# Optimization experiments

Measured on AMD Instinct MI355X. Metric: run time of the kernel, lower is better.

The kernel has to match this reference:

```python
import jax, jax.numpy as jnp
import numpy as np
import math

B, N, IN_DIM = 128, 100, 8
E, H, FF, L = 512, 8, 2048, 6
DH = E // H
MAX_STEPS = int(N * 1.5)
EPS = 1e-5

def _ln(x, g, b):
    mu = x.mean(-1, keepdims=True)
    var = ((x - mu) ** 2).mean(-1, keepdims=True)
    return (x - mu) / jnp.sqrt(var + EPS) * g + b

def _mha(q_in, k_in, v_in, wq, bq, wk, bk, wv, bv, wo, bo):
    Bq, Sq = q_in.shape[0], q_in.shape[1]
    q = (q_in @ wq + bq).reshape(Bq, Sq, H, DH)
    k = (k_in @ wk + bk).reshape(Bq, -1, H, DH)
    v = (v_in @ wv + bv).reshape(Bq, -1, H, DH)
    s = jnp.einsum('bqhd,bkhd->bhqk', q, k) / math.sqrt(DH)
    a = jax.nn.softmax(s, axis=-1)
    o = jnp.einsum('bhqk,bkhd->bqhd', a, v).reshape(Bq, Sq, E)
    return o @ wo + bo

def setup_inputs():
    key = jax.random.key(0)
    keys = iter(jax.random.split(key, 64))
    def nrm(shape, s=0.02):
        return jax.random.normal(next(keys), shape, jnp.float32) * s
    d = {}
    d['node_features'] = jax.random.normal(next(keys), (B, N, IN_DIM), jnp.float32)
    d['edge_weights'] = jax.random.uniform(next(keys), (B, N, N), jnp.float32)
    pos = np.arange(N)[:, None].astype(np.float32)
    div = np.exp(np.arange(0, E, 2).astype(np.float32) * (-math.log(10000.0) / E))
    pe = np.zeros((N, E), np.float32)
    pe[:, 0::2] = np.sin(pos * div); pe[:, 1::2] = np.cos(pos * div)
    d['pe'] = jnp.asarray(pe)
    d['in_w'] = nrm((IN_DIM, E)); d['in_b'] = jnp.zeros((E,), jnp.float32)
    for nm in ['enc_wq', 'enc_wk', 'enc_wv', 'enc_wo']:
        d[nm] = nrm((L, E, E))
    for nm in ['enc_bq', 'enc_bk', 'enc_bv', 'enc_bo']:
        d[nm] = jnp.zeros((L, E), jnp.float32)
    d['enc_w1'] = nrm((L, E, FF)); d['enc_b1'] = jnp.zeros((L, FF), jnp.float32)
    d['enc_w2'] = nrm((L, FF, E)); d['enc_b2'] = jnp.zeros((L, E), jnp.float32)
    d['enc_ln1g'] = jnp.ones((L, E), jnp.float32); d['enc_ln1b'] = jnp.zeros((L, E), jnp.float32)
    d['enc_ln2g'] = jnp.ones((L, E), jnp.float32); d['enc_ln2b'] = jnp.zeros((L, E), jnp.float32)
    d['lstm_wih'] = nrm((E, 4 * E)); d['lstm_whh'] = nrm((E, 4 * E))
    d['lstm_bih'] = jnp.zeros((4 * E,), jnp.float32); d['lstm_bhh'] = jnp.zeros((4 * E,), jnp.float32)
    for nm in ['dec_wq', 'dec_wk', 'dec_wv', 'dec_wo', 'dec_pw']:
        d[nm] = nrm((E, E))
    for nm in ['dec_bq', 'dec_bk', 'dec_bv', 'dec_bo', 'dec_pb']:
        d[nm] = jnp.zeros((E,), jnp.float32)
    d['dec_lng'] = jnp.ones((E,), jnp.float32); d['dec_lnb'] = jnp.zeros((E,), jnp.float32)
    d['shortcut_bonus'] = jnp.asarray(5.0, jnp.float32)
    d['revisit_penalty'] = jnp.asarray(-0.5, jnp.float32)
    d['done_w'] = nrm((E, 1)); d['done_b'] = jnp.zeros((1,), jnp.float32)
    return d

def _forward(node_features, edge_weights, pe, in_w, in_b, enc_wq, enc_bq, enc_wk, enc_bk, enc_wv, enc_bv, enc_wo, enc_bo, enc_w1, enc_b1, enc_w2, enc_b2, enc_ln1g, enc_ln1b, enc_ln2g, enc_ln2b, lstm_wih, lstm_whh, lstm_bih, lstm_bhh, dec_wq, dec_bq, dec_wk, dec_bk, dec_wv, dec_bv, dec_wo, dec_bo, dec_pw, dec_pb, dec_lng, dec_lnb, shortcut_bonus, revisit_penalty, done_w, done_b):
    # ---- Encoder (dropout = eval-mode identity) ----
    x = node_features @ in_w + in_b + pe[:N]
    for l in range(L):
        attn = _mha(x, x, x, enc_wq[l], enc_bq[l], enc_wk[l], enc_bk[l], enc_wv[l], enc_bv[l], enc_wo[l], enc_bo[l])
        x = _ln(x + attn, enc_ln1g[l], enc_ln1b[l])
        ff = jax.nn.relu(x @ enc_w1[l] + enc_b1[l]) @ enc_w2[l] + enc_b2[l]
        x = _ln(x + ff, enc_ln2g[l], enc_ln2b[l])
    node_emb = x  # [B, N, E]

    ar = jnp.arange(N)
    ew_to_first = edge_weights[:, :, 0]  # dist(mid -> node 0), [B, N]

    def step_fn(carry, step):
        h, c, ctx, visited, ucount, complete, all_vis, first, prev = carry
        # LSTMCell, torch gate order (i, f, g, o)
        gates = ctx @ lstm_wih + lstm_bih + h @ lstm_whh + lstm_bhh
        i_g, f_g, g_g, o_g = jnp.split(gates, 4, axis=-1)
        c2 = jax.nn.sigmoid(f_g) * c + jax.nn.sigmoid(i_g) * jnp.tanh(g_g)
        h2 = jax.nn.sigmoid(o_g) * jnp.tanh(c2)
        # greedy done-predictor: stop if sigmoid(logit) > 0.5 once tour can be closed
        done_p = jax.nn.sigmoid(h2 @ done_w + done_b)[:, 0]
        eligible = (~complete) & (ucount >= N) & (step >= N)
        complete = complete | (eligible & (done_p > 0.5))
        # DecoderStep: 1-query attention over node embeddings
        a = _mha(h2[:, None, :], node_emb, node_emb, dec_wq, dec_bq, dec_wk, dec_bk, dec_wv, dec_bv, dec_wo, dec_bo)[:, 0]
        a = _ln(a, dec_lng, dec_lnb)
        logits = a @ dec_pw + dec_pb
        scores = jnp.einsum('be,bne->bn', logits, node_emb)
        # revisit penalty while tour incomplete (vectorized masked_fill_)
        scores = jnp.where((~all_vis)[:, None] & visited, revisit_penalty, scores)
        # shortcut bonus once all nodes visited (vectorized gather over edge_weights)
        ew_prev = jnp.take_along_axis(edge_weights, prev[:, None, None], axis=1)[:, 0, :]  # [B, N] row dist(prev -> *)
        direct = ew_prev[:, :1]                      # dist(prev -> 0)
        via = ew_prev + ew_to_first                  # dist(prev -> mid) + dist(mid -> 0)
        bonus = jnp.where(via < direct, shortcut_bonus * (direct - via) / direct, 0.0)
        scores = scores + jnp.where(all_vis[:, None], bonus, 0.0)
        # completed tours: force return to first node
        scores = jnp.where(complete[:, None], -1e9, scores)
        scores = jnp.where(complete[:, None] & (ar[None, :] == first[:, None]), 100.0, scores)
        probs = jax.nn.softmax(scores, axis=1)
        curr = jnp.argmax(probs, axis=1).astype(jnp.int32)  # greedy selection
        logp = jnp.log(jnp.take_along_axis(probs, curr[:, None], 1)[:, 0] + 1e-10)
        first = jnp.where(step == 0, curr, first)
        # state updates (guarded by active, as in the torch per-batch loop)
        active = ~complete
        cur_mask = ar[None, :] == curr[:, None]
        newly = active & ~jnp.take_along_axis(visited, curr[:, None], 1)[:, 0]
        ucount = ucount + newly.astype(jnp.int32)
        visited = visited | (active[:, None] & cur_mask)
        all_vis = all_vis | (ucount >= N)
        ctx2 = jnp.take_along_axis(node_emb, curr[:, None, None], axis=1)[:, 0, :]
        return (h2, c2, ctx2, visited, ucount, complete, all_vis, first, curr), (curr, logp)

    carry0 = (jnp.zeros((B, E), jnp.float32), jnp.zeros((B, E), jnp.float32), node_emb.mean(1),
              jnp.zeros((B, N), bool), jnp.zeros((B,), jnp.int32),
              jnp.zeros((B,), bool), jnp.zeros((B,), bool),
              jnp.zeros((B,), jnp.int32), jnp.zeros((B,), jnp.int32))
    carry, (tours, logps) = jax.lax.scan(step_fn, carry0, jnp.arange(MAX_STEPS))
    complete, first = carry[5], carry[7]
    # final forced step (step == max_steps in torch): incomplete tours return to first node, logp = 0
    final_node = jnp.where(complete, jnp.int32(0), first)
    tours = jnp.concatenate([tours, final_node[None]], 0)                 # [MAX_STEPS+1, B]
    logps = jnp.concatenate([logps, jnp.zeros((1, B), jnp.float32)], 0)   # [MAX_STEPS+1, B]
    return logps, tours

def reference(node_features, edge_weights, pe, in_w, in_b, enc_wq, enc_bq, enc_wk, enc_bk, enc_wv, enc_bv, enc_wo, enc_bo, enc_w1, enc_b1, enc_w2, enc_b2, enc_ln1g, enc_ln1b, enc_ln2g, enc_ln2b, lstm_wih, lstm_whh, lstm_bih, lstm_bhh, dec_wq, dec_bq, dec_wk, dec_bk, dec_wv, dec_bv, dec_wo, dec_bo, dec_pw, dec_pb, dec_lng, dec_lnb, shortcut_bonus, revisit_penalty, done_w, done_b):
    return _forward(node_features, edge_weights, pe, in_w, in_b, enc_wq, enc_bq, enc_wk, enc_bk, enc_wv, enc_bv, enc_wo, enc_bo, enc_w1, enc_b1, enc_w2, enc_b2, enc_ln1g, enc_ln1b, enc_ln2g, enc_ln2b, lstm_wih, lstm_whh, lstm_bih, lstm_bhh, dec_wq, dec_bq, dec_wk, dec_bk, dec_wv, dec_bv, dec_wo, dec_bo, dec_pw, dec_pb, dec_lng, dec_lnb, shortcut_bonus, revisit_penalty, done_w, done_b)
```

## Files before the change

kernel.cpp:

```cpp
#include <hip/hip_runtime.h>
#include <math.h>

#define Bb 128
#define Nn 100
#define Ee 512
#define Hh 8
#define DHd 64
#define FFf 2048
#define Ll 6
#define STEPS 150

typedef _Float16 h8 __attribute__((ext_vector_type(8)));
typedef _Float16 h4 __attribute__((ext_vector_type(4)));
typedef float f4 __attribute__((ext_vector_type(4)));

template<bool RELU, bool BIAS, bool OUTF32, bool SPLITK>
__global__ __launch_bounds__(256) void mgemm_k(
    const _Float16* __restrict__ Ah, const _Float16* __restrict__ Al, int lda,
    const _Float16* __restrict__ Bh, const _Float16* __restrict__ Bl, int ldb,
    float* __restrict__ C, _Float16* __restrict__ Ch, _Float16* __restrict__ Cl,
    int ldc, const float* __restrict__ bias, int K, int kc, int Mtot)
{
  __shared__ _Float16 sm[4 * 5120];
  _Float16* sAh = sm;
  _Float16* sAl = sm + 5120;
  _Float16* sBh = sm + 10240;
  _Float16* sBl = sm + 15360;
  const int tid = threadIdx.x;
  const int m0 = blockIdx.y * 128, n0 = blockIdx.x * 128;
  const int k0 = SPLITK ? blockIdx.z * kc : 0;
  const int kEnd = SPLITK ? k0 + kc : K;
  const int lane = tid & 63, wave = tid >> 6;
  const int wm = wave >> 1, wn = wave & 1;
  const int m16 = lane & 15, kg = lane >> 4;
  f4 acc[4][4];
#pragma unroll
  for (int i = 0; i < 4; ++i)
#pragma unroll
    for (int j = 0; j < 4; ++j) acc[i][j] = (f4)0.f;

  for (int kt = k0; kt < kEnd; kt += 32) {
#pragma unroll
    for (int it = 0; it < 2; ++it) {
      int idx = tid + it * 256;
      int row = idx >> 2, g = idx & 3;
      int lo_ = row * 40 + g * 8;
      size_t ga = (size_t)(m0 + row) * lda + kt + g * 8;
      size_t gb = (size_t)(n0 + row) * ldb + kt + g * 8;
      *(h8*)(sAh + lo_) = *(const h8*)(Ah + ga);
      *(h8*)(sAl + lo_) = *(const h8*)(Al + ga);
      *(h8*)(sBh + lo_) = *(const h8*)(Bh + gb);
      *(h8*)(sBl + lo_) = *(const h8*)(Bl + gb);
    }
    __syncthreads();
    h8 a_h[4], a_l[4], b_h[4], b_l[4];
#pragma unroll
    for (int i = 0; i < 4; ++i) {
      int ro = (wm * 64 + i * 16 + m16) * 40 + kg * 8;
      int co = (wn * 64 + i * 16 + m16) * 40 + kg * 8;
      a_h[i] = *(const h8*)(sAh + ro);
      a_l[i] = *(const h8*)(sAl + ro);
      b_h[i] = *(const h8*)(sBh + co);
      b_l[i] = *(const h8*)(sBl + co);
    }
#pragma unroll
    for (int i = 0; i < 4; ++i)
#pragma unroll
      for (int j = 0; j < 4; ++j) {
        acc[i][j] = __builtin_amdgcn_mfma_f32_16x16x32_f16(a_h[i], b_h[j], acc[i][j], 0, 0, 0);
        acc[i][j] = __builtin_amdgcn_mfma_f32_16x16x32_f16(a_h[i], b_l[j], acc[i][j], 0, 0, 0);
        acc[i][j] = __builtin_amdgcn_mfma_f32_16x16x32_f16(a_l[i], b_h[j], acc[i][j], 0, 0, 0);
      }
    __syncthreads();
  }

  float* Cz = OUTF32 ? (C + (SPLITK ? (size_t)blockIdx.z * (size_t)Mtot * ldc : (size_t)0)) : C;
  int rb = m0 + wm * 64 + kg * 4;
  int cb = n0 + wn * 64 + m16;
#pragma unroll
  for (int j = 0; j < 4; ++j) {
    int col = cb + j * 16;
    float bv = BIAS ? bias[col] : 0.f;
#pragma unroll
    for (int i = 0; i < 4; ++i) {
#pragma unroll
      for (int r = 0; r < 4; ++r) {
        float v = acc[i][j][r] + bv;
        if (RELU) v = fmaxf(v, 0.f);
        int row = rb + i * 16 + r;
        if (OUTF32) {
          Cz[(size_t)row * ldc + col] = v;
        } else {
          _Float16 hh = (_Float16)v;
          Ch[(size_t)row * ldc + col] = hh;
          Cl[(size_t)row * ldc + col] = (_Float16)(v - (float)hh);
        }
      }
    }
  }
}

__global__ __launch_bounds__(256) void wconv_k(
    const float* __restrict__ W, int K, int N,
    _Float16* __restrict__ Th, _Float16* __restrict__ Tl)
{
  __shared__ float t[32][33];
  int n0 = blockIdx.x * 32, k0 = blockIdx.y * 32;
  int tid = threadIdx.x;
  int r = tid >> 3, c4 = (tid & 7) * 4;
  float4 v = *(const float4*)(W + (size_t)(k0 + r) * N + n0 + c4);
  t[r][c4 + 0] = v.x; t[r][c4 + 1] = v.y; t[r][c4 + 2] = v.z; t[r][c4 + 3] = v.w;
  __syncthreads();
  h4 hi, lo;
#pragma unroll
  for (int i = 0; i < 4; ++i) {
    float x = t[c4 + i][r];
    _Float16 hh = (_Float16)x;
    hi[i] = hh;
    lo[i] = (_Float16)(x - (float)hh);
  }
  *(h4*)(Th + (size_t)(n0 + r) * K + k0 + c4) = hi;
  *(h4*)(Tl + (size_t)(n0 + r) * K + k0 + c4) = lo;
}

__global__ __launch_bounds__(256) void reduce4_k(
    const float* __restrict__ P, const float* __restrict__ bias, float* __restrict__ out)
{
  int idx = blockIdx.x * 256 + threadIdx.x;
  const size_t S = 3200ull * 512;
  float v = P[idx] + P[idx + S] + P[idx + 2 * S] + P[idx + 3 * S] + bias[idx & 511];
  out[idx] = v;
}

__global__ __launch_bounds__(256) void input_proj_k(
    const float* __restrict__ nf, const float* __restrict__ inw,
    const float* __restrict__ inb, const float* __restrict__ pe,
    float* __restrict__ x, _Float16* __restrict__ xh, _Float16* __restrict__ xl)
{
  int idx = blockIdx.x * 256 + threadIdx.x;
  int bn = idx >> 9, e = idx & 511;
  int n = bn - (bn / Nn) * Nn;
  const float* fr = nf + (size_t)bn * 8;
  float s = inb[e] + pe[(size_t)n * 512 + e];
#pragma unroll
  for (int i = 0; i < 8; ++i) s += fr[i] * inw[(size_t)i * 512 + e];
  x[idx] = s;
  _Float16 hh = (_Float16)s;
  xh[idx] = hh;
  xl[idx] = (_Float16)(s - (float)hh);
}

__global__ __launch_bounds__(256) void ln_k(
    const float* __restrict__ xin, const float* __restrict__ yin,
    const float* __restrict__ g, const float* __restrict__ bb,
    float* __restrict__ out, _Float16* __restrict__ oh, _Float16* __restrict__ ol)
{
  int row = blockIdx.x, t = threadIdx.x;
  __shared__ float red[256];
  size_t base = (size_t)row * 512;
  float v0 = xin[base + t] + yin[base + t];
  float v1 = xin[base + 256 + t] + yin[base + 256 + t];
  red[t] = v0 + v1;
  __syncthreads();
  for (int o = 128; o > 0; o >>= 1) { if (t < o) red[t] += red[t + o]; __syncthreads(); }
  float mu = red[0] * (1.f / 512.f);
  __syncthreads();
  float d0 = v0 - mu, d1 = v1 - mu;
  red[t] = d0 * d0 + d1 * d1;
  __syncthreads();
  for (int o = 128; o > 0; o >>= 1) { if (t < o) red[t] += red[t + o]; __syncthreads(); }
  float inv = 1.f / sqrtf(red[0] * (1.f / 512.f) + 1e-5f);
  float y0 = d0 * inv * g[t] + bb[t];
  float y1 = d1 * inv * g[t + 256] + bb[t + 256];
  out[base + t] = y0;
  out[base + 256 + t] = y1;
// ... 45 lines not shown
#pragma unroll
    for (int c = 0; c < 7; ++c) {
      int i = i0 + r, j = j0 + c;
      if (i < Nn && j < Nn) p[i * 104 + j] = s[r][c] * 0.125f;
    }
  __syncthreads();
  int w = t >> 6, lane = t & 63;
  for (int i = w; i < Nn; i += 4) {
    float x0 = p[i * 104 + lane];
    float x1 = (lane < 36) ? p[i * 104 + 64 + lane] : -3.4e38f;
    float mx = fmaxf(x0, x1);
    for (int msk = 32; msk; msk >>= 1) mx = fmaxf(mx, __shfl_xor(mx, msk));
    float e0 = expf(x0 - mx);
    float e1 = (lane < 36) ? expf(x1 - mx) : 0.f;
    float ss = e0 + e1;
    for (int msk = 32; msk; msk >>= 1) ss += __shfl_xor(ss, msk);
    p[i * 104 + lane] = e0 / ss;
    if (lane < 36) p[i * 104 + 64 + lane] = e1 / ss;
  }
  __syncthreads();
  int d0 = tj * 4;
  float oa[7][4];
#pragma unroll
  for (int r = 0; r < 7; ++r)
#pragma unroll
    for (int c = 0; c < 4; ++c) oa[r][c] = 0.f;
  for (int j = 0; j < Nn; ++j) {
    float pr[7];
#pragma unroll
    for (int r = 0; r < 7; ++r) pr[r] = p[(i0 + r) * 104 + j];
    float4 vv = *(const float4*)(vg + (size_t)j * 512 + d0);
#pragma unroll
    for (int r = 0; r < 7; ++r) {
      oa[r][0] += pr[r] * vv.x; oa[r][1] += pr[r] * vv.y;
      oa[r][2] += pr[r] * vv.z; oa[r][3] += pr[r] * vv.w;
    }
  }
  size_t ob = ((size_t)b * Nn) * 512 + h * 64 + d0;
#pragma unroll
  for (int r = 0; r < 7; ++r)
    if (i0 + r < Nn) {
      h4 hv, lv;
#pragma unroll
      for (int c = 0; c < 4; ++c) {
        _Float16 hh = (_Float16)oa[r][c];
        hv[c] = hh;
        lv[c] = (_Float16)(oa[r][c] - (float)hh);
      }
      *(h4*)(oh + ob + (size_t)(i0 + r) * 512) = hv;
      *(h4*)(ol + ob + (size_t)(i0 + r) * 512) = lv;
    }
}

template<int BM, int BN, int BK, int TM, int TN>
__global__ __launch_bounds__(256) void gemm_k(
    const float* __restrict__ A, int lda,
    const float* __restrict__ B1, const float* __restrict__ B2, int splitB, int ldb,
    float* __restrict__ C, int ldc, int M, int N, int K, int kChunk)
{
  __shared__ __align__(16) float As[BK][BM + 4];
  __shared__ __align__(16) float Bs[BK][BN + 4];
  const int tid = threadIdx.x;
  const int m0 = blockIdx.y * BM;
  const int n0 = blockIdx.x * BN;
  const int k0 = blockIdx.z * kChunk;
  const int kEnd = k0 + kChunk;
  constexpr int TCOLS = BN / TN;
  const int tm = tid / TCOLS;
  const int tn = tid % TCOLS;
  float acc[TM][TN];
#pragma unroll
  for (int i = 0; i < TM; ++i)
#pragma unroll
    for (int j = 0; j < TN; ++j) acc[i][j] = 0.f;

  for (int kt = k0; kt < kEnd; kt += BK) {
    constexpr int A4 = BM * BK / 4;
    for (int c = tid; c < A4; c += 256) {
      int mm = c / (BK / 4);
      int k4 = (c % (BK / 4)) * 4;
      float4 av = *(const float4*)(A + (size_t)(m0 + mm) * lda + kt + k4);
      As[k4 + 0][mm] = av.x;
      As[k4 + 1][mm] = av.y;
      As[k4 + 2][mm] = av.z;
      As[k4 + 3][mm] = av.w;
    }
    constexpr int B4 = BK * BN / 4;
    for (int c = tid; c < B4; c += 256) {
      int kk = c / (BN / 4);
      int n4 = (c % (BN / 4)) * 4;
      int kgi = kt + kk;
      const float* Brow = (kgi < splitB) ? (B1 + (size_t)kgi * ldb)
                                         : (B2 + (size_t)(kgi - splitB) * ldb);
      *(float4*)&Bs[kk][n4] = *(const float4*)(Brow + n0 + n4);
    }
    __syncthreads();
#pragma unroll
    for (int kk = 0; kk < BK; ++kk) {
      float a[TM], b[TN];
#pragma unroll
      for (int i = 0; i < TM; ++i) a[i] = As[kk][tm * TM + i];
#pragma unroll
      for (int j = 0; j < TN; ++j) b[j] = Bs[kk][tn * TN + j];
#pragma unroll
      for (int i = 0; i < TM; ++i)
#pragma unroll
        for (int j = 0; j < TN; ++j)
          acc[i][j] += a[i] * b[j];
    }
    __syncthreads();
  }

  float* Cout = C + (size_t)blockIdx.z * (size_t)M * ldc;
#pragma unroll
  for (int i = 0; i < TM; ++i) {
    int m = m0 + tm * TM + i;
#pragma unroll
    for (int j = 0; j < TN; j += 4) {
      int n = n0 + tn * TN + j;
      float4 r;
      r.x = acc[i][j + 0]; r.y = acc[i][j + 1]; r.z = acc[i][j + 2]; r.w = acc[i][j + 3];
      *(float4*)(Cout + (size_t)m * ldc + n) = r;
    }
  }
}

__global__ __launch_bounds__(256) void init_k(
    const float* __restrict__ emb, float* __restrict__ ctxh, float* __restrict__ cbuf,
    int* visited, int* ucount, int* complete, int* allvis, int* first, int* prev,
    float* out)
{
  int b = blockIdx.x, t = threadIdx.x;
#pragma unroll
  for (int r = 0; r < 2; ++r) {
    int e = t + 256 * r;
    float s = 0.f;
    for (int i = 0; i < Nn; ++i) s += emb[((size_t)b * Nn + i) * 512 + e];
    ctxh[(size_t)b * 1024 + e] = s / 100.f;
    ctxh[(size_t)b * 1024 + 512 + e] = 0.f;
    cbuf[(size_t)b * 512 + e] = 0.f;
  }
  if (t < Nn) visited[b * Nn + t] = 0;
  if (t == 0) {
    ucount[b] = 0; complete[b] = 0; allvis[b] = 0; first[b] = 0; prev[b] = 0;
    out[150 * Bb + b] = 0.f;
  }
}

__device__ __forceinline__ float sigm(float x) { return 1.f / (1.f + expf(-x)); }

__global__ __launch_bounds__(256) void lstm_pw_k(
    const float* __restrict__ gP, const float* __restrict__ bih, const float* __restrict__ bhh,
    float* __restrict__ ctxh, float* __restrict__ cbuf,
    const float* __restrict__ done_w, const float* __restrict__ done_b,
    int* complete, const int* ucount, int step)
{
  int b = blockIdx.x, t = threadIdx.x;
  __shared__ float red[256];
  const float* g0 = gP + (size_t)b * 2048;
  const float* g1 = gP + 262144 + (size_t)b * 2048;
  float dsum = 0.f;
#pragma unroll
  for (int r = 0; r < 2; ++r) {
    int e = t + 256 * r;
    float ig = g0[e] + g1[e] + bih[e] + bhh[e];
    float fg = g0[e + 512] + g1[e + 512] + bih[e + 512] + bhh[e + 512];
    float gg = g0[e + 1024] + g1[e + 1024] + bih[e + 1024] + bhh[e + 1024];
    float og = g0[e + 1536] + g1[e + 1536] + bih[e + 1536] + bhh[e + 1536];
    float cprev = cbuf[(size_t)b * 512 + e];
    float c2 = sigm(fg) * cprev + sigm(ig) * tanhf(gg);
    float h2 = sigm(og) * tanhf(c2);
    cbuf[(size_t)b * 512 + e] = c2;
    ctxh[(size_t)b * 1024 + 512 + e] = h2;
    dsum += h2 * done_w[e];
  }
  red[t] = dsum; __syncthreads();
  for (int o = 128; o > 0; o >>= 1) { if (t < o) red[t] += red[t + o]; __syncthreads(); }
  if (t == 0) {
    float z = red[0] + done_b[0];
    if (!complete[b] && ucount[b] >= Nn && step >= Nn && z > 0.f) complete[b] = 1;
  }
}

__global__ __launch_bounds__(128) void dec_attn_k(
    const float* __restrict__ qP, const float* __restrict__ bq,
    const float* __restrict__ Kd, const float* __restrict__ Vd,
    float* __restrict__ o)
{
  int bh = blockIdx.x; int b = bh >> 3, h = bh & 7;
  int t = threadIdx.x;
  __shared__ float qh[64];
  __shared__ float p[100];
  __shared__ float red[128];
  if (t < 64) {
    float s = bq[h * 64 + t];
#pragma unroll
    for (int s8 = 0; s8 < 8; ++s8) s += qP[(size_t)s8 * 65536 + (size_t)b * 512 + h * 64 + t];
    qh[t] = s;
  }
  __syncthreads();
  float scv = -3.4e38f;
  if (t < Nn) {
    const float* kr = Kd + ((size_t)b * Nn + t) * 512 + h * 64;
    float s = 0.f;
#pragma unroll
    for (int d = 0; d < 64; ++d) s += qh[d] * kr[d];
    scv = s * 0.125f;
  }
  red[t] = scv; __syncthreads();
  for (int o2 = 64; o2 > 0; o2 >>= 1) { if (t < o2) red[t] = fmaxf(red[t], red[t + o2]); __syncthreads(); }
  float m = red[0]; __syncthreads();
  float ex = (t < Nn) ? expf(scv - m) : 0.f;
  red[t] = ex; __syncthreads();
  for (int o2 = 64; o2 > 0; o2 >>= 1) { if (t < o2) red[t] += red[t + o2]; __syncthreads(); }
  float Z = red[0];
  if (t < Nn) p[t] = ex / Z;
  __syncthreads();
  if (t < 64) {
    float acc = 0.f;
    const float* vr = Vd + (size_t)b * Nn * 512 + h * 64 + t;
    for (int j = 0; j < Nn; ++j) acc += p[j] * vr[(size_t)j * 512];
    o[(size_t)b * 512 + h * 64 + t] = acc;
  }
}

__global__ __launch_bounds__(256) void dec_ln_k(
    const float* __restrict__ woP, const float* __restrict__ bo,
    const float* __restrict__ g, const float* __restrict__ bb,
    float* __restrict__ out)
{
  int b = blockIdx.x, t = threadIdx.x;
  __shared__ float red[256];
  float v[2];
#pragma unroll
  for (int r = 0; r < 2; ++r) {
    int e = t + 256 * r;
    float s = bo[e];
#pragma unroll
    for (int s8 = 0; s8 < 8; ++s8) s += woP[(size_t)s8 * 65536 + (size_t)b * 512 + e];
    v[r] = s;
  }
  red[t] = v[0] + v[1]; __syncthreads();
  for (int o = 128; o > 0; o >>= 1) { if (t < o) red[t] += red[t + o]; __syncthreads(); }
  float mu = red[0] * (1.f / 512.f);
  __syncthreads();
  float d0 = v[0] - mu, d1 = v[1] - mu;
  red[t] = d0 * d0 + d1 * d1; __syncthreads();
  for (int o = 128; o > 0; o >>= 1) { if (t < o) red[t] += red[t + o]; __syncthreads(); }
  float inv = 1.f / sqrtf(red[0] * (1.f / 512.f) + 1e-5f);
  out[(size_t)b * 512 + t] = d0 * inv * g[t] + bb[t];
  out[(size_t)b * 512 + t + 256] = d1 * inv * g[t + 256] + bb[t + 256];
}

__global__ __launch_bounds__(256) void select_k(
    const float* __restrict__ pwP, const float* __restrict__ pb,
    const float* __restrict__ emb, const float* __restrict__ ew,
    int* visited, int* ucount, int* complete, int* allvis, int* first, int* prev,
    float* __restrict__ ctxh, float* __restrict__ out,
    const float* __restrict__ sb_p, const float* __restrict__ rp_p, int step)
{
  int b = blockIdx.x, t = threadIdx.x;
  __shared__ float logits[512];
  __shared__ float sc[128];
  __shared__ float red[256];
  __shared__ int redi[256];
#pragma unroll
  for (int r = 0; r < 2; ++r) {
    int e = t + 256 * r;
    float s = pb[e];
#pragma unroll
    for (int s8 = 0; s8 < 8; ++s8) s += pwP[(size_t)s8 * 65536 + (size_t)b * 512 + e];
    logits[e] = s;
  }
  __syncthreads();
  if (t < Nn) {
    const float* er = emb + ((size_t)b * Nn + t) * 512;
    float s = 0.f;
    for (int e = 0; e < 512; ++e) s += logits[e] * er[e];
    int av = allvis[b];
    if (!av && visited[b * Nn + t]) s = rp_p[0];
    if (av) {
      int pv = prev[b];
      float direct = ew[(size_t)b * 10000 + (size_t)pv * 100];
      float via = ew[(size_t)b * 10000 + (size_t)pv * 100 + t] + ew[(size_t)b * 10000 + (size_t)t * 100];
      if (via < direct) s += sb_p[0] * (direct - via) / direct;
    }
    if (complete[b]) s = (t == first[b]) ? 100.f : -1e9f;
    sc[t] = s;
  }
  __syncthreads();
  float vv = (t < Nn) ? sc[t] : -3.4e38f;
  int ii = (t < Nn) ? t : 0x7fffffff;
  red[t] = vv; redi[t] = ii;
  __syncthreads();
  for (int o = 128; o > 0; o >>= 1) {
    if (t < o) {
      float v2 = red[t + o]; int i2 = redi[t + o];
      if (v2 > red[t] || (v2 == red[t] && i2 < redi[t])) { red[t] = v2; redi[t] = i2; }
    }
    __syncthreads();
  }
  float m = red[0];
  int curr = redi[0];
  __syncthreads();
  float ex = (t < Nn) ? expf(sc[t] - m) : 0.f;
  red[t] = ex; __syncthreads();
  for (int o = 128; o > 0; o >>= 1) { if (t < o) red[t] += red[t + o]; __syncthreads(); }
  float Z = red[0];
  if (t == 0) {
    float pcur = expf(sc[curr] - m) / Z;
    out[step * Bb + b] = logf(pcur + 1e-10f);
    out[(151 + step) * Bb + b] = (float)curr;
    if (!complete[b]) {
      if (!visited[b * Nn + curr]) ucount[b] = ucount[b] + 1;
      visited[b * Nn + curr] = 1;
    }
    if (ucount[b] >= Nn) allvis[b] = 1;
    if (step == 0) first[b] = curr;
    prev[b] = curr;
  }
  const float* src = emb + ((size_t)b * Nn + curr) * 512;
  ctxh[(size_t)b * 1024 + t] = src[t];
  ctxh[(size_t)b * 1024 + t + 256] = src[t + 256];
}

__global__ void final_k(const int* complete, const int* first, float* out)
{
  int b = threadIdx.x;
  out[(151 + 150) * Bb + b] = complete[b] ? 0.f : (float)first[b];
}

extern "C" void kernel_launch(void* const* d_in, const int* in_sizes, int n_in,
                              void* d_out, int out_size, void* d_ws, size_t ws_size,
                              hipStream_t stream)
{
  const float* nf      = (const float*)d_in[0];
  const float* ew      = (const float*)d_in[1];
  const float* pe      = (const float*)d_in[2];
  const float* in_w    = (const float*)d_in[3];
  const float* in_b    = (const float*)d_in[4];
  const float* enc_wq  = (const float*)d_in[5];
  const float* enc_wk  = (const float*)d_in[6];
  const float* enc_wv  = (const float*)d_in[7];
  const float* enc_wo  = (const float*)d_in[8];
  const float* enc_bq  = (const float*)d_in[9];
  const float* enc_bk  = (const float*)d_in[10];
  const float* enc_bv  = (const float*)d_in[11];
  const float* enc_bo  = (const float*)d_in[12];
  const float* enc_w1  = (const float*)d_in[13];
  const float* enc_b1  = (const float*)d_in[14];
  const float* enc_w2  = (const float*)d_in[15];
  const float* enc_b2  = (const float*)d_in[16];
  const float* ln1g    = (const float*)d_in[17];
  const float* ln1b    = (const float*)d_in[18];
  const float* ln2g    = (const float*)d_in[19];
  const float* ln2b    = (const float*)d_in[20];
  const float* wih     = (const float*)d_in[21];
  const float* whh     = (const float*)d_in[22];
  const float* bih     = (const float*)d_in[23];
  const float* bhh     = (const float*)d_in[24];
  const float* dwq     = (const float*)d_in[25];
  const float* dwk     = (const float*)d_in[26];
  const float* dwv     = (const float*)d_in[27];
  const float* dwo     = (const float*)d_in[28];
  const float* dpw     = (const float*)d_in[29];
  const float* dbq     = (const float*)d_in[30];
  const float* dbk     = (const float*)d_in[31];
  const float* dbv     = (const float*)d_in[32];
  const float* dbo     = (const float*)d_in[33];
  const float* dpb     = (const float*)d_in[34];
  const float* dlng    = (const float*)d_in[35];
  const float* dlnb    = (const float*)d_in[36];
  const float* sbp     = (const float*)d_in[37];
  const float* rpp     = (const float*)d_in[38];
  const float* done_w  = (const float*)d_in[39];
  const float* done_b  = (const float*)d_in[40];
  float* out = (float*)d_out;

  const size_t SZ = 12800ull * 512;
  float* ws = (float*)d_ws;
  float* x   = ws;
  float* xq  = x + SZ;
  float* xk  = xq + SZ;
  float* xv  = xk + SZ;
  _Float16* xh = (_Float16*)(xv + SZ);
  _Float16* xl = xh + SZ;
  _Float16* oh = xl + SZ;
  _Float16* ol = oh + SZ;
  _Float16* wb = ol + SZ;
  _Float16* wqh = wb;               _Float16* wql = wqh + 262144;
  _Float16* wkh = wql + 262144;     _Float16* wkl = wkh + 262144;
  _Float16* wvh = wkl + 262144;     _Float16* wvl = wvh + 262144;
  _Float16* woh_ = wvl + 262144;    _Float16* wol_ = woh_ + 262144;
  _Float16* w1h = wol_ + 262144;    _Float16* w1l = w1h + 1048576;
  _Float16* w2h = w1l + 1048576;    _Float16* w2l = w2h + 1048576;
  float* ctxh   = (float*)(w2l + 1048576);
  float* cbuf   = ctxh + 131072;
  float* gatesP = cbuf + 65536;
  float* qP     = gatesP + 524288;
  float* woP    = qP + 524288;
  float* pwP    = woP + 524288;
  float* abuf   = pwP + 524288;
  float* dbuf   = abuf + 65536;
  int* ivis     = (int*)(dbuf + 65536);
  int* ucount   = ivis + 12800;
  int* complete = ucount + 128;
  int* allvis   = complete + 128;
  int* first    = allvis + 128;
  int* prev     = first + 128;

  input_proj_k<<<25600, 256, 0, stream>>>(nf, in_w, in_b, pe, x, xh, xl);

  for (int l = 0; l < Ll; ++l) {
    const float* wq = enc_wq + (size_t)l * 262144;
    const float* wk = enc_wk + (size_t)l * 262144;
    const float* wv = enc_wv + (size_t)l * 262144;
    const float* wo = enc_wo + (size_t)l * 262144;
    const float* bq = enc_bq + (size_t)l * 512;
    const float* bk = enc_bk + (size_t)l * 512;
    const float* bv = enc_bv + (size_t)l * 512;
    const float* bo = enc_bo + (size_t)l * 512;
    const float* w1 = enc_w1 + (size_t)l * 1048576;
    const float* b1 = enc_b1 + (size_t)l * 2048;
    const float* w2 = enc_w2 + (size_t)l * 1048576;
    const float* b2 = enc_b2 + (size_t)l * 512;

    wconv_k<<<dim3(16, 16), 256, 0, stream>>>(wq, 512, 512, wqh, wql);
    wconv_k<<<dim3(16, 16), 256, 0, stream>>>(wk, 512, 512, wkh, wkl);
    wconv_k<<<dim3(16, 16), 256, 0, stream>>>(wv, 512, 512, wvh, wvl);
    wconv_k<<<dim3(16, 16), 256, 0, stream>>>(wo, 512, 512, woh_, wol_);
    wconv_k<<<dim3(64, 16), 256, 0, stream>>>(w1, 512, 2048, w1h, w1l);
    wconv_k<<<dim3(16, 64), 256, 0, stream>>>(w2, 2048, 512, w2h, w2l);

    mgemm_k<false, true, true, false><<<dim3(4, 100), 256, 0, stream>>>(
        xh, xl, 512, wqh, wql, 512, xq, nullptr, nullptr, 512, bq, 512, 0, 0);
    mgemm_k<false, true, true, false><<<dim3(4, 100), 256, 0, stream>>>(
        xh, xl, 512, wkh, wkl, 512, xk, nullptr, nullptr, 512, bk, 512, 0, 0);
    mgemm_k<false, true, true, false><<<dim3(4, 100), 256, 0, stream>>>(
        xh, xl, 512, wvh, wvl, 512, xv, nullptr, nullptr, 512, bv, 512, 0, 0);
    enc_attn_k<<<1024, 256, 0, stream>>>(xq, xk, xv, oh, ol);
    mgemm_k<false, true, true, false><<<dim3(4, 100), 256, 0, stream>>>(
        oh, ol, 512, woh_, wol_, 512, xq, nullptr, nullptr, 512, bo, 512, 0, 0);
    ln_k<<<12800, 256, 0, stream>>>(x, xq, ln1g + l * 512, ln1b + l * 512, x, xh, xl);
    for (int c = 0; c < 4; ++c) {
      mgemm_k<true, true, false, false><<<dim3(16, 25), 256, 0, stream>>>(
          xh + (size_t)c * 3200 * 512, xl + (size_t)c * 3200 * 512, 512,
          w1h, w1l, 512, nullptr, oh, ol, 2048, b1, 512, 0, 0);
      mgemm_k<false, false, true, true><<<dim3(4, 25, 4), 256, 0, stream>>>(
          oh, ol, 2048, w2h, w2l, 2048, xv, nullptr, nullptr, 512,
          nullptr, 2048, 512, 3200);
      reduce4_k<<<6400, 256, 0, stream>>>(xv, b2, xq + (size_t)c * 3200 * 512);
    }
    ln_k<<<12800, 256, 0, stream>>>(x, xq, ln2g + l * 512, ln2b + l * 512, x, xh, xl);
  }

  wconv_k<<<dim3(16, 16), 256, 0, stream>>>(dwk, 512, 512, wqh, wql);
  wconv_k<<<dim3(16, 16), 256, 0, stream>>>(dwv, 512, 512, wkh, wkl);
  mgemm_k<false, true, true, false><<<dim3(4, 100), 256, 0, stream>>>(
      xh, xl, 512, wqh, wql, 512, xk, nullptr, nullptr, 512, dbk, 512, 0, 0);
  mgemm_k<false, true, true, false><<<dim3(4, 100), 256, 0, stream>>>(
      xh, xl, 512, wkh, wkl, 512, xv, nullptr, nullptr, 512, dbv, 512, 0, 0);
  init_k<<<128, 256, 0, stream>>>(x, ctxh, cbuf, ivis, ucount, complete, allvis, first, prev, out);

  for (int step = 0; step < STEPS; ++step) {
    gemm_k<32, 64, 16, 2, 4><<<dim3(32, 4, 2), 256, 0, stream>>>(
        ctxh, 1024, wih, whh, 512, 2048, gatesP, 2048, 128, 2048, 1024, 512);
    lstm_pw_k<<<128, 256, 0, stream>>>(gatesP, bih, bhh, ctxh, cbuf, done_w, done_b,
                                       complete, ucount, step);
    gemm_k<32, 64, 16, 2, 4><<<dim3(8, 4, 8), 256, 0, stream>>>(
        ctxh + 512, 1024, dwq, dwq, 1 << 30, 512, qP, 512, 128, 512, 512, 64);
    dec_attn_k<<<1024, 128, 0, stream>>>(qP, dbq, xk, xv, dbuf);
    gemm_k<32, 64, 16, 2, 4><<<dim3(8, 4, 8), 256, 0, stream>>>(
        dbuf, 512, dwo, dwo, 1 << 30, 512, woP, 512, 128, 512, 512, 64);
    dec_ln_k<<<128, 256, 0, stream>>>(woP, dbo, dlng, dlnb, abuf);
    gemm_k<32, 64, 16, 2, 4><<<dim3(8, 4, 8), 256, 0, stream>>>(
        abuf, 512, dpw, dpw, 1 << 30, 512, pwP, 512, 128, 512, 512, 64);
    select_k<<<128, 256, 0, stream>>>(pwP, dpb, x, ew, ivis, ucount, complete, allvis,
                                      first, prev, ctxh, out, sbp, rpp, step);
  }
  final_k<<<1, 128, 0, stream>>>(complete, first, out);
}
```

Measured before the change: 16.51 ms.

## Fuse decoder step into three kernels with MFMA LSTM and precomputed pointer projection

Collapses the per-step decoder pipeline from eight launches to three. The LSTM gate GEMM now runs on split-fp16 MFMA with the gate weights pre-transposed and interleaved, so each block owns the four gates of its columns and applies the pointwise update itself. The query projection and attention are merged into one kernel. The out-projection, layer norm and pointer selection are merged into another, and the pointer projection is algebraically moved onto the embeddings once (emb·W^T plus a bias term) before the loop. This removes split-K partial buffers and launch overhead. In exchange it adds some precomputation, and the fused matvecs run on few blocks with serial k-loops.

```diff
diff --git a/kernel.cpp b/kernel.cpp
--- a/kernel.cpp
+++ b/kernel.cpp
@@ -29,7 +29,7 @@
   const int tid = threadIdx.x;
   const int m0 = blockIdx.y * 128, n0 = blockIdx.x * 128;
   const int k0 = SPLITK ? blockIdx.z * kc : 0;
-  const int kEnd = SPLITK ? k0 + kc : K;
+  const int kEnd = SPLITK ? (k0 + kc) : K;
   const int lane = tid & 63, wave = tid >> 6;
   const int wm = wave >> 1, wn = wave & 1;
   const int m16 = lane & 15, kg = lane >> 4;
@@ -121,6 +121,36 @@
   }
   *(h4*)(Th + (size_t)(n0 + r) * K + k0 + c4) = hi;
   *(h4*)(Tl + (size_t)(n0 + r) * K + k0 + c4) = lo;
+}
+
+__global__ __launch_bounds__(256) void wconvg_k(
+    const float* __restrict__ Wa, const float* __restrict__ Wb,
+    _Float16* __restrict__ Th, _Float16* __restrict__ Tl)
+{
+  int np = blockIdx.x;
+  int j = np >> 4, q = (np >> 2) & 3, r = np & 3;
+  int n = q * 512 + j * 4 + r;
+  int t = threadIdx.x;
+#pragma unroll
+  for (int kk = 0; kk < 4; ++kk) {
+    int k = t + kk * 256;
+    float x = (k < 512) ? Wa[(size_t)k * 2048 + n] : Wb[(size_t)(k - 512) * 2048 + n];
+    _Float16 hh = (_Float16)x;
+    Th[(size_t)np * 1024 + k] = hh;
+    Tl[(size_t)np * 1024 + k] = (_Float16)(x - (float)hh);
+  }
+}
+
+__global__ __launch_bounds__(256) void wsplit_k(
+    const float* __restrict__ W, _Float16* __restrict__ Th, _Float16* __restrict__ Tl, int n)
+{
+  int i = blockIdx.x * 256 + threadIdx.x;
+  if (i < n) {
+    float x = W[i];
+    _Float16 hh = (_Float16)x;
+    Th[i] = hh;
+    Tl[i] = (_Float16)(x - (float)hh);
+  }
 }
 
 __global__ __launch_bounds__(256) void reduce4_k(
@@ -272,81 +302,21 @@
     }
 }
 
-template<int BM, int BN, int BK, int TM, int TN>
-__global__ __launch_bounds__(256) void gemm_k(
-    const float* __restrict__ A, int lda,
-    const float* __restrict__ B1, const float* __restrict__ B2, int splitB, int ldb,
-    float* __restrict__ C, int ldc, int M, int N, int K, int kChunk)
-{
-  __shared__ __align__(16) float As[BK][BM + 4];
-  __shared__ __align__(16) float Bs[BK][BN + 4];
-  const int tid = threadIdx.x;
-  const int m0 = blockIdx.y * BM;
-  const int n0 = blockIdx.x * BN;
-  const int k0 = blockIdx.z * kChunk;
-  const int kEnd = k0 + kChunk;
-  constexpr int TCOLS = BN / TN;
-  const int tm = tid / TCOLS;
-  const int tn = tid % TCOLS;
-  float acc[TM][TN];
-#pragma unroll
-  for (int i = 0; i < TM; ++i)
-#pragma unroll
-    for (int j = 0; j < TN; ++j) acc[i][j] = 0.f;
-
-  for (int kt = k0; kt < kEnd; kt += BK) {
-    constexpr int A4 = BM * BK / 4;
-    for (int c = tid; c < A4; c += 256) {
-      int mm = c / (BK / 4);
-      int k4 = (c % (BK / 4)) * 4;
-      float4 av = *(const float4*)(A + (size_t)(m0 + mm) * lda + kt + k4);
-      As[k4 + 0][mm] = av.x;
-      As[k4 + 1][mm] = av.y;
-      As[k4 + 2][mm] = av.z;
-      As[k4 + 3][mm] = av.w;
-    }
-    constexpr int B4 = BK * BN / 4;
-    for (int c = tid; c < B4; c += 256) {
-      int kk = c / (BN / 4);
-      int n4 = (c % (BN / 4)) * 4;
-      int kgi = kt + kk;
-      const float* Brow = (kgi < splitB) ? (B1 + (size_t)kgi * ldb)
-                                         : (B2 + (size_t)(kgi - splitB) * ldb);
-      *(float4*)&Bs[kk][n4] = *(const float4*)(Brow + n0 + n4);
-    }
-    __syncthreads();
-#pragma unroll
-    for (int kk = 0; kk < BK; ++kk) {
-      float a[TM], b[TN];
-#pragma unroll
-      for (int i = 0; i < TM; ++i) a[i] = As[kk][tm * TM + i];
-#pragma unroll
-      for (int j = 0; j < TN; ++j) b[j] = Bs[kk][tn * TN + j];
-#pragma unroll
-      for (int i = 0; i < TM; ++i)
-#pragma unroll
-        for (int j = 0; j < TN; ++j)
-          acc[i][j] += a[i] * b[j];
-    }
-    __syncthreads();
-  }
-
-  float* Cout = C + (size_t)blockIdx.z * (size_t)M * ldc;
-#pragma unroll
-  for (int i = 0; i < TM; ++i) {
-    int m = m0 + tm * TM + i;
-#pragma unroll
-    for (int j = 0; j < TN; j += 4) {
-      int n = n0 + tn * TN + j;
-      float4 r;
-      r.x = acc[i][j + 0]; r.y = acc[i][j + 1]; r.z = acc[i][j + 2]; r.w = acc[i][j + 3];
-      *(float4*)(Cout + (size_t)m * ldc + n) = r;
-    }
-  }
-}
-
-__global__ __launch_bounds__(256) void init_k(
-    const float* __restrict__ emb, float* __restrict__ ctxh, float* __restrict__ cbuf,
+__global__ __launch_bounds__(256) void sb2_k(
+    const float* __restrict__ emb, const float* __restrict__ dpb, float* __restrict__ sb2)
+{
+  int m = blockIdx.x * 4 + (threadIdx.x >> 6);
+  int lane = threadIdx.x & 63;
+  const float* er = emb + (size_t)m * 512;
+  float s = 0.f;
+  for (int e = lane; e < 512; e += 64) s += dpb[e] * er[e];
+  for (int msk = 32; msk; msk >>= 1) s += __shfl_xor(s, msk);
+  if (lane == 0) sb2[m] = s;
+}
+
+__global__ __launch_bounds__(256) void init2_k(
+    const float* __restrict__ emb, _Float16* __restrict__ ctxph, _Float16* __restrict__ ctxpl,
+    float* __restrict__ ctxh, float* __restrict__ cbuf,
     int* visited, int* ucount, int* complete, int* allvis, int* first, int* prev,
     float* out)
 {
@@ -356,7 +326,12 @@
     int e = t + 256 * r;
     float s = 0.f;
     for (int i = 0; i < Nn; ++i) s += emb[((size_t)b * Nn + i) * 512 + e];
-    ctxh[(size_t)b * 1024 + e] = s / 100.f;
+    s *= (1.f / 100.f);
+    _Float16 hh = (_Float16)s;
+    ctxph[b * 1024 + e] = hh;
+    ctxpl[b * 1024 + e] = (_Float16)(s - (float)hh);
+    ctxph[b * 1024 + 512 + e] = (_Float16)0.f;
+    ctxpl[b * 1024 + 512 + e] = (_Float16)0.f;
     ctxh[(size_t)b * 1024 + 512 + e] = 0.f;
     cbuf[(size_t)b * 512 + e] = 0.f;
   }
@@ -369,97 +344,195 @@
 
 __device__ __forceinline__ float sigm(float x) { return 1.f / (1.f + expf(-x)); }
 
-__global__ __launch_bounds__(256) void lstm_pw_k(
-    const float* __restrict__ gP, const float* __restrict__ bih, const float* __restrict__ bhh,
-    float* __restrict__ ctxh, float* __restrict__ cbuf,
-    const float* __restrict__ done_w, const float* __restrict__ done_b,
-    int* complete, const int* ucount, int step)
-{
-  int b = blockIdx.x, t = threadIdx.x;
+__global__ __launch_bounds__(256) void ph1_k(
+    const _Float16* __restrict__ ctxph, const _Float16* __restrict__ ctxpl,
+    const _Float16* __restrict__ WgTh, const _Float16* __restrict__ WgTl,
+    const float* __restrict__ bih, const float* __restrict__ bhh,
+    float* __restrict__ cbuf, float* __restrict__ ctxh,
+    _Float16* __restrict__ hph, _Float16* __restrict__ hpl,
+    const float* __restrict__ done_w, float* __restrict__ ddp)
+{
+  __shared__ __align__(16) _Float16 sm[11520];
+  __shared__ __align__(16) float gt[128 * 17];
+  _Float16* sAh = sm;
+  _Float16* sAl = sm + 5120;
+  _Float16* sBh = sm + 10240;
+  _Float16* sBl = sm + 10880;
+  const int j = blockIdx.x, t = threadIdx.x;
+  const int lane = t & 63, wave = t >> 6;
+  const int m16 = lane & 15, kg = lane >> 4;
+  f4 acc[2];
+  acc[0] = (f4)0.f; acc[1] = (f4)0.f;
+
+  for (int kt = 0; kt < 1024; kt += 32) {
+#pragma unroll
+    for (int it = 0; it < 2; ++it) {
+      int idx = t + it * 256;
+      int row = idx >> 2, g = idx & 3;
+      int lo_ = row * 40 + g * 8;
+      size_t ga = (size_t)row * 1024 + kt + g * 8;
+      *(h8*)(sAh + lo_) = *(const h8*)(ctxph + ga);
+      *(h8*)(sAl + lo_) = *(const h8*)(ctxpl + ga);
+    }
+    if (t < 64) {
+      int row = t >> 2, g = t & 3;
+      int lo_ = row * 40 + g * 8;
+      size_t gb = (size_t)(j * 16 + row) * 1024 + kt + g * 8;
+      *(h8*)(sBh + lo_) = *(const h8*)(WgTh + gb);
+      *(h8*)(sBl + lo_) = *(const h8*)(WgTl + gb);
+    }
+    __syncthreads();
+    h8 b_h = *(const h8*)(sBh + m16 * 40 + kg * 8);
+    h8 b_l = *(const h8*)(sBl + m16 * 40 + kg * 8);
+#pragma unroll
+    for (int i = 0; i < 2; ++i) {
+      int ro = ((wave * 2 + i) * 16 + m16) * 40 + kg * 8;
+      h8 a_h = *(const h8*)(sAh + ro);
+      h8 a_l = *(const h8*)(sAl + ro);
+      acc[i] = __builtin_amdgcn_mfma_f32_16x16x32_f16(a_h, b_h, acc[i], 0, 0, 0);
+      acc[i] = __builtin_amdgcn_mfma_f32_16x16x32_f16(a_h, b_l, acc[i], 0, 0, 0);
+      acc[i] = __builtin_amdgcn_mfma_f32_16x16x32_f16(a_l, b_h, acc[i], 0, 0, 0);
+    }
+    __syncthreads();
+  }
+#pragma unroll
+  for (int i = 0; i < 2; ++i) {
+    int base = (wave * 2 + i) * 16 + kg * 4;
+#pragma unroll
+    for (int r = 0; r < 4; ++r)
+      gt[(base + r) * 17 + m16] = acc[i][r];
+  }
+  __syncthreads();
+  if (t < 128) {
+    int b = t;
+    float dsum = 0.f;
+#pragma unroll
+    for (int r = 0; r < 4; ++r) {
+      int e = j * 4 + r;
+      float ig = gt[b * 17 + 0 + r]  + bih[e]        + bhh[e];
+      float fg = gt[b * 17 + 4 + r]  + bih[512 + e]  + bhh[512 + e];
+      float gg = gt[b * 17 + 8 + r]  + bih[1024 + e] + bhh[1024 + e];
+      float og = gt[b * 17 + 12 + r] + bih[1536 + e] + bhh[1536 + e];
+      float cprev = cbuf[(size_t)b * 512 + e];
+      float c2 = sigm(fg) * cprev + sigm(ig) * tanhf(gg);
+      float h2 = sigm(og) * tanhf(c2);
+      cbuf[(size_t)b * 512 + e] = c2;
+      ctxh[(size_t)b * 1024 + 512 + e] = h2;
+      _Float16 hh = (_Float16)h2;
+      hph[b * 1024 + 512 + e] = hh;
+      hpl[b * 1024 + 512 + e] = (_Float16)(h2 - (float)hh);
+      dsum += h2 * done_w[e];
+    }
+    ddp[b * 128 + j] = dsum;
+  }
+}
+
+__global__ __launch_bounds__(256) void ph2_k(
+    const float* __restrict__ ctxh, const float* __restrict__ dwq,
+    const float* __restrict__ dbq,
+    const float* __restrict__ Kd, const float* __restrict__ Vd,
+    float* __restrict__ obuf)
+{
+  __shared__ float hbuf[8][512];
+  __shared__ float qbuf[8][64];
+  __shared__ float sc2[2][320];
+  const int j = blockIdx.x, t = threadIdx.x;
+  const int h = j & 7, b0 = (j >> 3) * 8;
+  for (int i = t; i < 4096; i += 256) {
+    int bi = i >> 9, k = i & 511;
+    hbuf[bi][k] = ctxh[(size_t)(b0 + bi) * 1024 + 512 + k];
+  }
+  __syncthreads();
+  {
+    int d = t & 63, bi = t >> 6;
+    const float* wcol = dwq + h * 64 + d;
+#pragma unroll 1
+    for (int batch = 0; batch < 2; ++batch) {
+      int bb = batch * 4 + bi;
+      float s = 0.f;
+      for (int k = 0; k < 512; ++k) s += hbuf[bb][k] * wcol[(size_t)k * 512];
+      qbuf[bb][d] = s + dbq[h * 64 + d];
+    }
+  }
+  __syncthreads();
+  {
+    int half = t >> 7, tl = t & 127;
+    float* pv = sc2[half];
+    float* red = pv + 128;
+#pragma unroll 1
+    for (int r4 = 0; r4 < 4; ++r4) {
+      int item = r4 * 2 + half;
+      int b = b0 + item;
+      float scv = -3.4e38f;
+      if (tl < Nn) {
+        const float* kr = Kd + ((size_t)(b * Nn + tl)) * 512 + h * 64;
+        float s = 0.f;
+#pragma unroll
+        for (int d = 0; d < 64; ++d) s += qbuf[item][d] * kr[d];
+        scv = s * 0.125f;
+      }
+      red[tl] = scv; __syncthreads();
+      for (int o2 = 64; o2 > 0; o2 >>= 1) { if (tl < o2) red[tl] = fmaxf(red[tl], red[tl + o2]); __syncthreads(); }
+      float m = red[0]; __syncthreads();
+      float ex = (tl < Nn) ? expf(scv - m) : 0.f;
+      red[tl] = ex; __syncthreads();
+      for (int o2 = 64; o2 > 0; o2 >>= 1) { if (tl < o2) red[tl] += red[tl + o2]; __syncthreads(); }
+      float Z = red[0];
+      if (tl < Nn) pv[tl] = ex / Z;
+      __syncthreads();
+      if (tl < 64) {
+        float acc = 0.f;
+        const float* vr = Vd + (size_t)(b * Nn) * 512 + h * 64 + tl;
+        for (int jj = 0; jj < Nn; ++jj) acc += pv[jj] * vr[(size_t)jj * 512];
+        obuf[(size_t)b * 512 + h * 64 + tl] = acc;
+      }
+      __syncthreads();
+    }
+  }
+}
+
+__global__ __launch_bounds__(256) void ph3_k(
+    const float* __restrict__ ddp, const float* __restrict__ done_b,
+    const float* __restrict__ obuf, const float* __restrict__ dwo,
+    const float* __restrict__ dbo, const float* __restrict__ dlng,
+    const float* __restrict__ dlnb,
+    const float* __restrict__ M2, const float* __restrict__ sb2,
+    const float* __restrict__ ew, const float* __restrict__ sbp,
+    const float* __restrict__ rpp,
+    const _Float16* __restrict__ embh, const _Float16* __restrict__ embl,
+    int* visited, int* ucount, int* complete, int* allvis, int* first, int* prev,
+    _Float16* __restrict__ ctxph, _Float16* __restrict__ ctxpl,
+    float* __restrict__ out, int step)
+{
+  __shared__ float ob[512];
+  __shared__ float av[512];
   __shared__ float red[256];
-  const float* g0 = gP + (size_t)b * 2048;
-  const float* g1 = gP + 262144 + (size_t)b * 2048;
-  float dsum = 0.f;
-#pragma unroll
-  for (int r = 0; r < 2; ++r) {
-    int e = t + 256 * r;
-    float ig = g0[e] + g1[e] + bih[e] + bhh[e];
-    float fg = g0[e + 512] + g1[e + 512] + bih[e + 512] + bhh[e + 512];
-    float gg = g0[e + 1024] + g1[e + 1024] + bih[e + 1024] + bhh[e + 1024];
-    float og = g0[e + 1536] + g1[e + 1536] + bih[e + 1536] + bhh[e + 1536];
-    float cprev = cbuf[(size_t)b * 512 + e];
-    float c2 = sigm(fg) * cprev + sigm(ig) * tanhf(gg);
-    float h2 = sigm(og) * tanhf(c2);
-    cbuf[(size_t)b * 512 + e] = c2;
-    ctxh[(size_t)b * 1024 + 512 + e] = h2;
-    dsum += h2 * done_w[e];
-  }
-  red[t] = dsum; __syncthreads();
+  __shared__ int redi[256];
+  __shared__ float sc[128];
+  __shared__ int cflag;
+  const int b = blockIdx.x, t = threadIdx.x;
+  red[t] = (t < 128) ? ddp[b * 128 + t] : 0.f;
+  __syncthreads();
   for (int o = 128; o > 0; o >>= 1) { if (t < o) red[t] += red[t + o]; __syncthreads(); }
   if (t == 0) {
     float z = red[0] + done_b[0];
-    if (!complete[b] && ucount[b] >= Nn && step >= Nn && z > 0.f) complete[b] = 1;
-  }
-}
-
-__global__ __launch_bounds__(128) void dec_attn_k(
-    const float* __restrict__ qP, const float* __restrict__ bq,
-    const float* __restrict__ Kd, const float* __restrict__ Vd,
-    float* __restrict__ o)
-{
-  int bh = blockIdx.x; int b = bh >> 3, h = bh & 7;
-  int t = threadIdx.x;
-  __shared__ float qh[64];
-  __shared__ float p[100];
-  __shared__ float red[128];
-  if (t < 64) {
-    float s = bq[h * 64 + t];
-#pragma unroll
-    for (int s8 = 0; s8 < 8; ++s8) s += qP[(size_t)s8 * 65536 + (size_t)b * 512 + h * 64 + t];
-    qh[t] = s;
-  }
-  __syncthreads();
-  float scv = -3.4e38f;
-  if (t < Nn) {
-    const float* kr = Kd + ((size_t)b * Nn + t) * 512 + h * 64;
-    float s = 0.f;
-#pragma unroll
-    for (int d = 0; d < 64; ++d) s += qh[d] * kr[d];
-    scv = s * 0.125f;
-  }
-  red[t] = scv; __syncthreads();
-  for (int o2 = 64; o2 > 0; o2 >>= 1) { if (t < o2) red[t] = fmaxf(red[t], red[t + o2]); __syncthreads(); }
-  float m = red[0]; __syncthreads();
-  float ex = (t < Nn) ? expf(scv - m) : 0.f;
-  red[t] = ex; __syncthreads();
-  for (int o2 = 64; o2 > 0; o2 >>= 1) { if (t < o2) red[t] += red[t + o2]; __syncthreads(); }
-  float Z = red[0];
-  if (t < Nn) p[t] = ex / Z;
-  __syncthreads();
-  if (t < 64) {
-    float acc = 0.f;
-    const float* vr = Vd + (size_t)b * Nn * 512 + h * 64 + t;
-    for (int j = 0; j < Nn; ++j) acc += p[j] * vr[(size_t)j * 512];
-    o[(size_t)b * 512 + h * 64 + t] = acc;
-  }
-}
-
-__global__ __launch_bounds__(256) void dec_ln_k(
-    const float* __restrict__ woP, const float* __restrict__ bo,
-    const float* __restrict__ g, const float* __restrict__ bb,
-    float* __restrict__ out)
-{
-  int b = blockIdx.x, t = threadIdx.x;
-  __shared__ float red[256];
+    int c = complete[b];
+    if (!c && ucount[b] >= Nn && step >= Nn && z > 0.f) { c = 1; complete[b] = 1; }
+    cflag = c;
+  }
+  ob[t] = obuf[(size_t)b * 512 + t];
+  ob[t + 256] = obuf[(size_t)b * 512 + t + 256];
+  __syncthreads();
   float v[2];
 #pragma unroll
   for (int r = 0; r < 2; ++r) {
-    int e = t + 256 * r;
-    float s = bo[e];
-#pragma unroll
-    for (int s8 = 0; s8 < 8; ++s8) s += woP[(size_t)s8 * 65536 + (size_t)b * 512 + e];
+    int col = t + r * 256;
+    float s = dbo[col];
+    const float* wcol = dwo + col;
+    for (int k = 0; k < 512; ++k) s += ob[k] * wcol[(size_t)k * 512];
     v[r] = s;
   }
+  __syncthreads();
   red[t] = v[0] + v[1]; __syncthreads();
   for (int o = 128; o > 0; o >>= 1) { if (t < o) red[t] += red[t + o]; __syncthreads(); }
   float mu = red[0] * (1.f / 512.f);
@@ -468,44 +541,23 @@
   red[t] = d0 * d0 + d1 * d1; __syncthreads();
   for (int o = 128; o > 0; o >>= 1) { if (t < o) red[t] += red[t + o]; __syncthreads(); }
   float inv = 1.f / sqrtf(red[0] * (1.f / 512.f) + 1e-5f);
-  out[(size_t)b * 512 + t] = d0 * inv * g[t] + bb[t];
-  out[(size_t)b * 512 + t + 256] = d1 * inv * g[t + 256] + bb[t + 256];
-}
-
-__global__ __launch_bounds__(256) void select_k(
-    const float* __restrict__ pwP, const float* __restrict__ pb,
-    const float* __restrict__ emb, const float* __restrict__ ew,
-    int* visited, int* ucount, int* complete, int* allvis, int* first, int* prev,
-    float* __restrict__ ctxh, float* __restrict__ out,
-    const float* __restrict__ sb_p, const float* __restrict__ rp_p, int step)
-{
-  int b = blockIdx.x, t = threadIdx.x;
-  __shared__ float logits[512];
-  __shared__ float sc[128];
-  __shared__ float red[256];
-  __shared__ int redi[256];
-#pragma unroll
-  for (int r = 0; r < 2; ++r) {
-    int e = t + 256 * r;
-    float s = pb[e];
-#pragma unroll
-    for (int s8 = 0; s8 < 8; ++s8) s += pwP[(size_t)s8 * 65536 + (size_t)b * 512 + e];
-    logits[e] = s;
-  }
+  av[t] = d0 * inv * dlng[t] + dlnb[t];
+  av[t + 256] = d1 * inv * dlng[t + 256] + dlnb[t + 256];
   __syncthreads();
   if (t < Nn) {
-    const float* er = emb + ((size_t)b * Nn + t) * 512;
-    float s = 0.f;
-    for (int e = 0; e < 512; ++e) s += logits[e] * er[e];
-    int av = allvis[b];
-    if (!av && visited[b * Nn + t]) s = rp_p[0];
-    if (av) {
-      int pv = prev[b];
-      float direct = ew[(size_t)b * 10000 + (size_t)pv * 100];
-      float via = ew[(size_t)b * 10000 + (size_t)pv * 100 + t] + ew[(size_t)b * 10000 + (size_t)t * 100];
-      if (via < direct) s += sb_p[0] * (direct - via) / direct;
-    }
-    if (complete[b]) s = (t == first[b]) ? 100.f : -1e9f;
+    const float* m2r = M2 + ((size_t)(b * Nn + t)) * 512;
+    float s = sb2[b * Nn + t];
+    for (int jj = 0; jj < 512; ++jj) s += av[jj] * m2r[jj];
+    int avz = allvis[b];
+    if (!avz && visited[b * Nn + t]) s = rpp[0];
+    if (avz) {
+      int pvn = prev[b];
+      float direct = ew[(size_t)b * 10000 + (size_t)pvn * 100];
+      float via = ew[(size_t)b * 10000 + (size_t)pvn * 100 + t]
+                + ew[(size_t)b * 10000 + (size_t)t * 100];
+      if (via < direct) s += sbp[0] * (direct - via) / direct;
+    }
+    if (cflag) s = (t == first[b]) ? 100.f : -1e9f;
     sc[t] = s;
   }
   __syncthreads();
@@ -531,7 +583,7 @@
     float pcur = expf(sc[curr] - m) / Z;
     out[step * Bb + b] = logf(pcur + 1e-10f);
     out[(151 + step) * Bb + b] = (float)curr;
-    if (!complete[b]) {
+    if (!cflag) {
       if (!visited[b * Nn + curr]) ucount[b] = ucount[b] + 1;
       visited[b * Nn + curr] = 1;
     }
@@ -539,9 +591,11 @@
     if (step == 0) first[b] = curr;
     prev[b] = curr;
   }
-  const float* src = emb + ((size_t)b * Nn + curr) * 512;
-  ctxh[(size_t)b * 1024 + t] = src[t];
-  ctxh[(size_t)b * 1024 + t + 256] = src[t + 256];
+  size_t src = ((size_t)(b * Nn) + (size_t)curr) * 512;
+  ctxph[b * 1024 + t]       = embh[src + t];
+  ctxph[b * 1024 + t + 256] = embh[src + t + 256];
+  ctxpl[b * 1024 + t]       = embl[src + t];
+  ctxpl[b * 1024 + t + 256] = embl[src + t + 256];
 }
 
 __global__ void final_k(const int* complete, const int* first, float* out)
@@ -614,20 +668,21 @@
   _Float16* woh_ = wvl + 262144;    _Float16* wol_ = woh_ + 262144;
   _Float16* w1h = wol_ + 262144;    _Float16* w1l = w1h + 1048576;
   _Float16* w2h = w1l + 1048576;    _Float16* w2l = w2h + 1048576;
-  float* ctxh   = (float*)(w2l + 1048576);
+  float* tail   = (float*)(w2l + 1048576);
+  float* sb2    = tail;
+  float* ddp    = sb2 + 12800;
+  float* obuf   = ddp + 16384;
+  float* ctxh   = obuf + 65536;
   float* cbuf   = ctxh + 131072;
-  float* gatesP = cbuf + 65536;
-  float* qP     = gatesP + 524288;
-  float* woP    = qP + 524288;
-  float* pwP    = woP + 524288;
-  float* abuf   = pwP + 524288;
-  float* dbuf   = abuf + 65536;
-  int* ivis     = (int*)(dbuf + 65536);
+  _Float16* ctxph = (_Float16*)(cbuf + 65536);
+  _Float16* ctxpl = ctxph + 131072;
+  int* ivis     = (int*)(ctxpl + 131072);
   int* ucount   = ivis + 12800;
   int* complete = ucount + 128;
   int* allvis   = complete + 128;
   int* first    = allvis + 128;
   int* prev     = first + 128;
+  float* M2 = xq;
 
   input_proj_k<<<25600, 256, 0, stream>>>(nf, in_w, in_b, pe, x, xh, xl);
 
@@ -680,23 +735,26 @@
       xh, xl, 512, wqh, wql, 512, xk, nullptr, nullptr, 512, dbk, 512, 0, 0);
   mgemm_k<false, true, true, false><<<dim3(4, 100), 256, 0, stream>>>(
       xh, xl, 512, wkh, wkl, 512, xv, nullptr, nullptr, 512, dbv, 512, 0, 0);
-  init_k<<<128, 256, 0, stream>>>(x, ctxh, cbuf, ivis, ucount, complete, allvis, first, prev, out);
+  _Float16* WgTh = wb;
+  _Float16* WgTl = WgTh + 2097152;
+  _Float16* dpwNh = WgTl + 2097152;
+  _Float16* dpwNl = dpwNh + 262144;
+  wconvg_k<<<2048, 256, 0, stream>>>(wih, whh, WgTh, WgTl);
+  wsplit_k<<<1024, 256, 0, stream>>>(dpw, dpwNh, dpwNl, 262144);
+  mgemm_k<false, false, true, false><<<dim3(4, 100), 256, 0, stream>>>(
+      xh, xl, 512, dpwNh, dpwNl, 512, M2, nullptr, nullptr, 512, nullptr, 512, 0, 0);
+  sb2_k<<<3200, 256, 0, stream>>>(x, dpb, sb2);
+  init2_k<<<128, 256, 0, stream>>>(x, ctxph, ctxpl, ctxh, cbuf, ivis, ucount,
+                                   complete, allvis, first, prev, out);
 
   for (int step = 0; step < STEPS; ++step) {
-    gemm_k<32, 64, 16, 2, 4><<<dim3(32, 4, 2), 256, 0, stream>>>(
-        ctxh, 1024, wih, whh, 512, 2048, gatesP, 2048, 128, 2048, 1024, 512);
-    lstm_pw_k<<<128, 256, 0, stream>>>(gatesP, bih, bhh, ctxh, cbuf, done_w, done_b,
-                                       complete, ucount, step);
-    gemm_k<32, 64, 16, 2, 4><<<dim3(8, 4, 8), 256, 0, stream>>>(
-        ctxh + 512, 1024, dwq, dwq, 1 << 30, 512, qP, 512, 128, 512, 512, 64);
-    dec_attn_k<<<1024, 128, 0, stream>>>(qP, dbq, xk, xv, dbuf);
-    gemm_k<32, 64, 16, 2, 4><<<dim3(8, 4, 8), 256, 0, stream>>>(
-        dbuf, 512, dwo, dwo, 1 << 30, 512, woP, 512, 128, 512, 512, 64);
-    dec_ln_k<<<128, 256, 0, stream>>>(woP, dbo, dlng, dlnb, abuf);
-    gemm_k<32, 64, 16, 2, 4><<<dim3(8, 4, 8), 256, 0, stream>>>(
-        abuf, 512, dpw, dpw, 1 << 30, 512, pwP, 512, 128, 512, 512, 64);
-    select_k<<<128, 256, 0, stream>>>(pwP, dpb, x, ew, ivis, ucount, complete, allvis,
-                                      first, prev, ctxh, out, sbp, rpp, step);
+    ph1_k<<<128, 256, 0, stream>>>(ctxph, ctxpl, WgTh, WgTl, bih, bhh,
+                                   cbuf, ctxh, ctxph, ctxpl, done_w, ddp);
+    ph2_k<<<128, 256, 0, stream>>>(ctxh, dwq, dbq, xk, xv, obuf);
+    ph3_k<<<128, 256, 0, stream>>>(ddp, done_b, obuf, dwo, dbo, dlng, dlnb,
+                                   M2, sb2, ew, sbp, rpp, xh, xl,
+                                   ivis, ucount, complete, allvis, first, prev,
+                                   ctxph, ctxpl, out, step);
   }
   final_k<<<1, 128, 0, stream>>>(complete, first, out);
 }
```

Result: slower. 21.29 ms (+29.0%).
